# Kernel optimization log

Hardware: AMD Instinct MI355X
Metric: run time of the kernel (lower is better)

## Reference

```python
import jax, jax.numpy as jnp
import numpy as np

# BERT-base geometry
B, N, H, DH = 4, 512, 12, 64
HID = H * DH            # 768
E = 65536               # total edges (~avg degree 32)
NREL = 64               # relation vocabulary


def setup_inputs() -> dict:
    key = jax.random.key(0)
    ks = jax.random.split(key, 12)
    node_states = jax.random.normal(ks[0], (B, N, HID), jnp.float32)
    b = jax.random.randint(ks[1], (E,), 0, B)
    hn = jax.random.randint(ks[2], (E,), 0, N)
    tn = jax.random.randint(ks[3], (E,), 0, N)
    r = jax.random.randint(ks[4], (E,), 0, NREL)
    edge_indices = jnp.stack([b, hn, tn, r]).astype(jnp.int32)  # (4, E)
    node_type_ids = jnp.zeros((B, N), jnp.int32)  # unused by this subclass
    sc = 0.02
    Wq = jax.random.normal(ks[5], (HID, HID), jnp.float32) * sc
    bq = jnp.zeros((HID,), jnp.float32)
    Wk = jax.random.normal(ks[6], (HID, HID), jnp.float32) * sc
    bk = jnp.zeros((HID,), jnp.float32)
    Wv = jax.random.normal(ks[7], (HID, HID), jnp.float32) * sc
    bv = jnp.zeros((HID,), jnp.float32)
    # relation matrix embeddings: one (DH, DH) matrix per relation id
    rel_emb = jnp.eye(DH, dtype=jnp.float32)[None] + jax.random.normal(ks[8], (NREL, DH, DH), jnp.float32) * sc
    return {"node_states": node_states, "edge_indices": edge_indices,
            "node_type_ids": node_type_ids, "Wq": Wq, "bq": bq,
            "Wk": Wk, "bk": bk, "Wv": Wv, "bv": bv, "rel_emb": rel_emb}


def reference(node_states, edge_indices, node_type_ids, Wq, bq, Wk, bk, Wv, bv, rel_emb):
    Bq, Nn, hid = node_states.shape
    # dense QKV projections (torch Linear: y = x @ W^T + b)
    Q = node_states @ Wq.T + bq
    K = node_states @ Wk.T + bk
    V = (node_states @ Wv.T + bv).reshape(Bq, Nn, H, DH)  # (B,N,H,D)
    be, he, te, re = edge_indices  # each (E,)
    # per-edge gathers
    Qe = Q[be, he].reshape(-1, H, DH)   # (E,H,D)
    Ke = K[be, te].reshape(-1, H, DH)   # (E,H,D)
    Re = rel_emb[re]                     # (E,D,D) relation matrix per edge
    # Q projected through relation matrix, then inner product with K per head
    Qp = jnp.einsum('ehd,edk->ehk', Qe, Re)
    logits = jnp.einsum('ehd,ehd->eh', Qp, Ke) / jnp.sqrt(jnp.float32(DH))  # (E,H)
    # sparse softmax over tail nodes: segment = (batch, head_node)
    seg = be * Nn + he
    nseg = Bq * Nn
    m = jax.ops.segment_max(logits, seg, num_segments=nseg)      # (BN,H)
    ex = jnp.exp(logits - m[seg])
    denom = jax.ops.segment_sum(ex, seg, num_segments=nseg)      # (BN,H)
    p = ex / denom[seg]                                          # (E,H)
    # dropout prob = 0.0 (deterministic reference)
    # aggregate: out[b,i,h,:] = sum_edges p_e * V[b, tail_e, h, :]
    contrib = p[:, :, None] * V[be, te]                          # (E,H,D)
    out = jax.ops.segment_sum(contrib, seg, num_segments=nseg)   # (BN,H,D)
    return out.reshape(Bq, Nn, H * DH)
```

## Files before the change

kernel.cpp:

```cpp
#include <hip/hip_runtime.h>
#include <hip/hip_bf16.h>

#define NB   4
#define NN   512
#define NH   12
#define DHD  64
#define HID  768
#define NE   65536
#define NSEG 2048
#define NREL 64
#define NSUB 32
#define NRSUB (NREL * NSUB)
#define LGS  16
#define POISON 0xAAAAAAAAu

typedef short bf16x8 __attribute__((ext_vector_type(8)));
typedef float f32x4  __attribute__((ext_vector_type(4)));
typedef unsigned short u16x8 __attribute__((ext_vector_type(8)));

__device__ __forceinline__ unsigned short f2bf(float f) {
    __hip_bfloat16 h = __float2bfloat16(f);
    return *reinterpret_cast<unsigned short*>(&h);
}
__device__ __forceinline__ float bf2f(unsigned short s) {
    return __int_as_float(((int)s) << 16);
}
__device__ __forceinline__ int unpz(int v) {
    return (int)((unsigned)v - POISON);
}
__device__ __forceinline__ void load_lds16(const void* g, void* l) {
    __builtin_amdgcn_global_load_lds(
        (const __attribute__((address_space(1))) unsigned int*)g,
        (__attribute__((address_space(3))) unsigned int*)l, 16, 0, 0);
}

#define NX4 ((2048 * 768) / 4)
#define NW4 ((768 * 768) / 4)
#define NCAST ((NX4 + 3 * NW4) / 256)
__global__ __launch_bounds__(256) void cast_hist_kernel(
    const float* __restrict__ X, const float* __restrict__ Wq,
    const float* __restrict__ Wk, const float* __restrict__ Wv,
    unsigned short* __restrict__ Xh, unsigned short* __restrict__ Wh,
    const int* __restrict__ ei,
    int* __restrict__ count, int* __restrict__ rcount2)
{
    if (blockIdx.x >= NCAST) {
        const int e = (blockIdx.x - NCAST) * 256 + threadIdx.x;
        const int b  = ei[e];
        const int hn = ei[NE + e];
        const int rr = ei[3 * NE + e];
        const int sub = (e >> 8) & (NSUB - 1);
        atomicAdd(&count[b * NN + hn], 1);
        atomicAdd(&rcount2[rr * NSUB + sub], 1);
        return;
    }
    const int i = blockIdx.x * 256 + threadIdx.x;
    float4 v;
    ushort4* dst;
    if (i < NX4) {
        v = ((const float4*)X)[i];
        dst = &((ushort4*)Xh)[i];
    } else {
        const int j = i - NX4;
        const float* W = (j < NW4) ? Wq : ((j < 2 * NW4) ? Wk : Wv);
        const int jj = (j < NW4) ? j : ((j < 2 * NW4) ? j - NW4 : j - 2 * NW4);
        v = ((const float4*)W)[jj];
        dst = &((ushort4*)Wh)[j];
    }
    ushort4 r;
    r.x = f2bf(v.x); r.y = f2bf(v.y); r.z = f2bf(v.z); r.w = f2bf(v.w);
    *dst = r;
}

#define NQKV 576
__global__ __launch_bounds__(256) void qkv_scatter_kernel(
    const unsigned short* __restrict__ Xh, const unsigned short* __restrict__ Wh,
    const float* __restrict__ bq, const float* __restrict__ bk,
    const float* __restrict__ bv,
    unsigned short* __restrict__ Qh, unsigned short* __restrict__ Kh,
    unsigned short* __restrict__ Vh,
    const int* __restrict__ ei,
    const int* __restrict__ count, const int* __restrict__ rcount2,
    int* __restrict__ cursor, int* __restrict__ rcursor2,
    int* __restrict__ s_te, int* __restrict__ s_pk, int* __restrict__ r_pos,
    int* __restrict__ offs_g, int* __restrict__ rofs2_g)
{
    __shared__ __align__(16) char smem[64 * 132 * 4];
    const int tid = threadIdx.x;

    if (blockIdx.x >= NQKV) {
        int* offs_l = (int*)smem;
        int* rofs_l = offs_l + NSEG;
        int* buf    = rofs_l + NRSUB;
        int* extra  = buf + 256;

        {
            int local[8];
            int s = 0;
            #pragma unroll
            for (int i = 0; i < 8; ++i) { local[i] = unpz(count[tid * 8 + i]); s += local[i]; }
            buf[tid] = s;
            __syncthreads();
            for (int off = 1; off < 256; off <<= 1) {
                const int v = (tid >= off) ? buf[tid - off] : 0;
                __syncthreads();
                buf[tid] += v;
                __syncthreads();
            }
            int run = buf[tid] - s;
            #pragma unroll
            for (int i = 0; i < 8; ++i) { offs_l[tid * 8 + i] = run; run += local[i]; }
            if (tid == 255) extra[0] = run;
            __syncthreads();
        }
        {
            int local[8];
            int s = 0;
            #pragma unroll
            for (int i = 0; i < 8; ++i) { local[i] = unpz(rcount2[tid * 8 + i]); s += local[i]; }
            buf[tid] = s;
            __syncthreads();
            for (int off = 1; off < 256; off <<= 1) {
                const int v = (tid >= off) ? buf[tid - off] : 0;
                __syncthreads();
                buf[tid] += v;
                __syncthreads();
            }
            int run = buf[tid] - s;
            #pragma unroll
            for (int i = 0; i < 8; ++i) { rofs_l[tid * 8 + i] = run; run += local[i]; }
            if (blockIdx.x == NQKV && tid == 255) rofs2_g[NRSUB] = run;
        }
        __syncthreads();

        if (blockIdx.x == NQKV) {
            #pragma unroll
            for (int i = 0; i < 8; ++i) {
                offs_g[tid * 8 + i]  = offs_l[tid * 8 + i];
                rofs2_g[tid * 8 + i] = rofs_l[tid * 8 + i];
            }
            if (tid == 255) offs_g[NSEG] = extra[0];
        }

        const int e = (blockIdx.x - NQKV) * 256 + tid;
        const int b  = ei[e];
        const int hn = ei[NE + e];
        const int tn = ei[2 * NE + e];
        const int rr = ei[3 * NE + e];
        const int sub = (e >> 8) & (NSUB - 1);
        const int seg = b * NN + hn;
        const int pos = offs_l[seg] + unpz(atomicAdd(&cursor[seg], 1));
        s_te[pos] = tn;
        s_pk[pos] = (seg << 9) | tn;
        const int rb = rr * NSUB + sub;
        const int rj = unpz(atomicAdd(&rcursor2[rb], 1));
        r_pos[rofs_l[rb] + rj] = pos;
        return;
    }

    const int bid = blockIdx.x;
    const int z   = bid / 192;
    const int rem = bid - z * 192;
    const int by  = rem / 6;
    const int bx  = rem - by * 6;
    const unsigned short* W = Wh + (size_t)z * (768 * 768);
    const float* bias = (z == 0) ? bq : ((z == 1) ? bk : bv);

    const int n0 = bx * 128;
    const int m0 = by * 64;
    const int lane = tid & 63;
    const int wave = tid >> 6;
    const int wm = wave >> 1, wn = wave & 1;

    unsigned short* As = (unsigned short*)smem;
    unsigned short* Bs = (unsigned short*)(smem + 8192);
    float* Cs = (float*)smem;

    f32x4 acc[2][4];
    #pragma unroll
    for (int a = 0; a < 2; ++a)
        #pragma unroll
        for (int b2 = 0; b2 < 4; ++b2) acc[a][b2] = (f32x4){0.f, 0.f, 0.f, 0.f};

    const int ml = lane & 15;
    const int q4 = lane >> 4;

    for (int k0 = 0; k0 < HID; k0 += 64) {
        __syncthreads();
        #pragma unroll
        for (int i = 0; i < 2; ++i) {
            const int slotb = i * 256 + wave * 64;
            const int idx = slotb + lane;
            const int row = idx >> 3;
            const int kq  = (idx & 7) ^ (row & 7);
            load_lds16(Xh + (size_t)(m0 + row) * HID + k0 + kq * 8,
                       As + slotb * 8);
        }
        #pragma unroll
        for (int i = 0; i < 4; ++i) {
            const int slotb = i * 256 + wave * 64;
            const int idx = slotb + lane;
            const int row = idx >> 3;
            const int kq  = (idx & 7) ^ (row & 7);
            load_lds16(W + (size_t)(n0 + row) * HID + k0 + kq * 8,
                       Bs + slotb * 8);
        }
        __syncthreads();

        #pragma unroll
        for (int ks = 0; ks < 2; ++ks) {
            bf16x8 af[2], bfr[4];
            #pragma unroll
            for (int t = 0; t < 2; ++t) {
                const int ar = wm * 32 + t * 16 + ml;
                const int ac = (ks * 4 + q4) ^ (ar & 7);
                af[t] = *(const bf16x8*)(As + ar * 64 + ac * 8);
            }
            #pragma unroll
            for (int t = 0; t < 4; ++t) {
                const int br = wn * 64 + t * 16 + ml;
                const int bc = (ks * 4 + q4) ^ (br & 7);
                bfr[t] = *(const bf16x8*)(Bs + br * 64 + bc * 8);
            }
            #pragma unroll
            for (int mt = 0; mt < 2; ++mt)
                #pragma unroll
                for (int nt = 0; nt < 4; ++nt)
                    acc[mt][nt] = __builtin_amdgcn_mfma_f32_16x16x32_bf16(
                        af[mt], bfr[nt], acc[mt][nt], 0, 0, 0);
        }
    }

    __syncthreads();
    #pragma unroll
    for (int mt = 0; mt < 2; ++mt)
        #pragma unroll
        for (int nt = 0; nt < 4; ++nt)
            #pragma unroll
            for (int rg = 0; rg < 4; ++rg)
                Cs[(wm * 32 + mt * 16 + q4 * 4 + rg) * 132 +
                   wn * 64 + nt * 16 + ml] = acc[mt][nt][rg];
    __syncthreads();

    unsigned short* Y = (z == 0) ? Qh : ((z == 1) ? Kh : Vh);
    #pragma unroll
    for (int it = 0; it < 4; ++it) {
        const int id  = tid + it * 256;
        const int row = id >> 4;
        const int cg  = id & 15;
        const float* cp = Cs + row * 132 + cg * 8;
        const float4 cA = *(const float4*)cp;
        const float4 cB = *(const float4*)(cp + 4);
        const float* bp = bias + n0 + cg * 8;
        const float4 bA = *(const float4*)bp;
        const float4 bB = *(const float4*)(bp + 4);
        const size_t o = (size_t)(m0 + row) * HID + n0 + cg * 8;
        u16x8 r;
        r[0] = f2bf(cA.x + bA.x); r[1] = f2bf(cA.y + bA.y);
        r[2] = f2bf(cA.z + bA.z); r[3] = f2bf(cA.w + bA.w);
        r[4] = f2bf(cB.x + bB.x); r[5] = f2bf(cB.y + bB.y);
        r[6] = f2bf(cB.z + bB.z); r[7] = f2bf(cB.w + bB.w);
        *(u16x8*)&Y[o] = r;
    }
}

#define RLY 32
__global__ __launch_bounds__(256) void rel_logits(
    const unsigned short* __restrict__ Qh, const unsigned short* __restrict__ Kh,
    const float* __restrict__ rel,
    const int* __restrict__ rofs2, const int* __restrict__ r_pos,
    const int* __restrict__ s_pk,
    float* __restrict__ Lg)
{
    const int r = blockIdx.x;
    const int rstart = rofs2[r * NSUB];
    const int rows = (rofs2[(r + 1) * NSUB] - rstart) * NH;
    if ((int)blockIdx.y * 256 >= rows) return;
    const int tid = threadIdx.x;
    const int lane = tid & 63;
    const int wave = tid >> 6;

    __shared__ int qb[256], kb[256], oi[256];
    __shared__ float QpS[4][16][68];

    bf16x8 bfrag[2][4];
    {
        const float* Rg = rel + (size_t)r * 4096;
        const int q4 = lane >> 4, n = lane & 15;
        #pragma unroll
        for (int ks = 0; ks < 2; ++ks)
            #pragma unroll
            for (int nt = 0; nt < 4; ++nt) {
                bf16x8 f;
                #pragma unroll
                for (int j = 0; j < 8; ++j)
                    f[j] = (short)f2bf(Rg[(ks * 32 + q4 * 8 + j) * 64 + nt * 16 + n]);
                bfrag[ks][nt] = f;
            }
    }

    for (int t0 = blockIdx.y * 256; t0 < rows; t0 += RLY * 256) {
        __syncthreads();
        {
            const int rowid = t0 + tid;
            if (rowid < rows) {
                const int el = rowid / 12;
                const int h  = rowid - el * 12;
                const int pos = r_pos[rstart + el];
                const int pk  = s_pk[pos];
                const int seg = pk >> 9;
                const int te  = pk & (NN - 1);
                qb[tid] = seg * HID + h * 64;
                kb[tid] = ((seg & ~(NN - 1)) + te) * HID + h * 64;
                oi[tid] = pos * LGS + h;
            } else { qb[tid] = 0; kb[tid] = 0; oi[tid] = -1; }
        }
        __syncthreads();

        for (int g = wave; g < 16; g += 4) {
            const int m = lane & 15, q4 = lane >> 4;
            const int qbase = qb[g * 16 + m];
            f32x4 cfr[4] = {{0,0,0,0},{0,0,0,0},{0,0,0,0},{0,0,0,0}};
            #pragma unroll
            for (int ks = 0; ks < 2; ++ks) {
                const bf16x8 afr = *(const bf16x8*)(Qh + qbase + ks * 32 + q4 * 8);
                #pragma unroll
                for (int nt = 0; nt < 4; ++nt)
                    cfr[nt] = __builtin_amdgcn_mfma_f32_16x16x32_bf16(
                        afr, bfrag[ks][nt], cfr[nt], 0, 0, 0);
            }
            #pragma unroll
            for (int nt = 0; nt < 4; ++nt)
                #pragma unroll
                for (int rg = 0; rg < 4; ++rg)
                    QpS[wave][q4 * 4 + rg][nt * 16 + m] = cfr[nt][rg];

            const int rw = lane >> 2, ch = (lane & 3) * 16;
            const int rowid2 = g * 16 + rw;
            const int kbase = kb[rowid2];
            const bf16x8 k0 = *(const bf16x8*)(Kh + kbase + ch);
            const bf16x8 k1 = *(const bf16x8*)(Kh + kbase + ch + 8);
            float s = 0.f;
            #pragma unroll
            for (int i = 0; i < 8; ++i) {
                s = fmaf(QpS[wave][rw][ch + i],     bf2f((unsigned short)k0[i]), s);
                s = fmaf(QpS[wave][rw][ch + 8 + i], bf2f((unsigned short)k1[i]), s);
            }
            s += __shfl_xor(s, 1, 64);
            s += __shfl_xor(s, 2, 64);
            if ((lane & 3) == 0) {
                const int o = oi[rowid2];
                if (o >= 0) Lg[o] = __expf(s * 0.125f);
            }
        }
    }
}

__global__ __launch_bounds__(256) void seg_softmax_agg(
    const unsigned short* __restrict__ Vh, const float* __restrict__ Lg,
    const int* __restrict__ offs, const int* __restrict__ s_te,
    float* __restrict__ out)
{
    const int seg  = blockIdx.x;
    const int tid  = threadIdx.x;
    const int lane = tid & 63;
    const int w    = tid >> 6;
    const int start = offs[seg];
    const int cnt   = offs[seg + 1] - start;
    const int browbase = seg & ~(NN - 1);

    __shared__ int   te_s[64];
    __shared__ float pv[4][3][64];

    float l0 = 0.f, l1 = 0.f, l2 = 0.f;
    float acc0 = 0.f, acc1 = 0.f, acc2 = 0.f;

    for (int c0 = 0; c0 < cnt; c0 += 64) {
        const int cc = min(64, cnt - c0);
        __syncthreads();
        if (tid < cc) te_s[tid] = s_te[start + c0 + tid];
        __syncthreads();

        float p0 = 0.f, p1 = 0.f, p2 = 0.f;
        if (lane < cc) {
            const float* Lp = Lg + (size_t)(start + c0 + lane) * LGS;
            p0 = Lp[w]; p1 = Lp[4 + w]; p2 = Lp[8 + w];
        }
        float s0 = p0, s1 = p1, s2 = p2;
        #pragma unroll
        for (int o = 1; o < 64; o <<= 1) {
            s0 += __shfl_xor(s0, o, 64);
            s1 += __shfl_xor(s1, o, 64);
            s2 += __shfl_xor(s2, o, 64);
        }
        l0 += s0; l1 += s1; l2 += s2;
        pv[w][0][lane] = p0; pv[w][1][lane] = p1; pv[w][2][lane] = p2;

        for (int j = 0; j < cc; ++j) {
            const unsigned short* __restrict__ Vr =
                Vh + (size_t)(browbase + te_s[j]) * HID + lane;
            acc0 = fmaf(pv[w][0][j], bf2f(Vr[w * 64]),       acc0);
            acc1 = fmaf(pv[w][1][j], bf2f(Vr[(4 + w) * 64]), acc1);
            acc2 = fmaf(pv[w][2][j], bf2f(Vr[(8 + w) * 64]), acc2);
        }
    }

    float* Yo = out + (size_t)seg * HID;
    Yo[tid]       = (l0 > 0.f) ? acc0 / l0 : 0.f;
    Yo[tid + 256] = (l1 > 0.f) ? acc1 / l1 : 0.f;
    Yo[tid + 512] = (l2 > 0.f) ? acc2 / l2 : 0.f;
}

extern "C" void kernel_launch(void* const* d_in, const int* in_sizes, int n_in,
                              void* d_out, int out_size, void* d_ws, size_t ws_size,
                              hipStream_t stream)
{
    const float* X   = (const float*)d_in[0];
    const int*   EI  = (const int*)d_in[1];
    const float* Wq  = (const float*)d_in[3];
    const float* bq  = (const float*)d_in[4];
    const float* Wk  = (const float*)d_in[5];
    const float* bk  = (const float*)d_in[6];
    const float* Wv  = (const float*)d_in[7];
    const float* bv  = (const float*)d_in[8];
    const float* rel = (const float*)d_in[9];
    float* out = (float*)d_out;

    char* p = (char*)d_ws;
    unsigned short* Qh = (unsigned short*)p;  p += (size_t)NSEG * HID * 2;
    unsigned short* Kh = (unsigned short*)p;  p += (size_t)NSEG * HID * 2;
    unsigned short* Vh = (unsigned short*)p;  p += (size_t)NSEG * HID * 2;
    unsigned short* Xh = (unsigned short*)p;
    float* Lg = (float*)p;                    p += (size_t)NE * LGS * 4;
    unsigned short* Wh = (unsigned short*)p;  p += (size_t)3 * 768 * 768 * 2;
    int* offs     = (int*)p;                  p += 2052 * 4;
    int* rofs2    = (int*)p;                  p += (NRSUB + 4) * 4;
    int* count    = (int*)p;                  p += NSEG * 4;
    int* cursor   = (int*)p;                  p += NSEG * 4;
    int* rcount2  = (int*)p;                  p += NRSUB * 4;
    int* rcursor2 = (int*)p;                  p += NRSUB * 4;
    int* s_te     = (int*)p;                  p += NE * 4;
    int* s_pk     = (int*)p;                  p += NE * 4;
    int* r_pos    = (int*)p;                  p += NE * 4;

    cast_hist_kernel<<<NCAST + 256, 256, 0, stream>>>(
        X, Wq, Wk, Wv, Xh, Wh, EI, count, rcount2);
    qkv_scatter_kernel<<<NQKV + 256, 256, 0, stream>>>(
        Xh, Wh, bq, bk, bv, Qh, Kh, Vh,
        EI, count, rcount2, cursor, rcursor2, s_te, s_pk, r_pos, offs, rofs2);
    rel_logits<<<dim3(NREL, RLY), 256, 0, stream>>>(Qh, Kh, rel, rofs2, r_pos,
                                                    s_pk, Lg);
    seg_softmax_agg<<<NSEG, 256, 0, stream>>>(Vh, Lg, offs, s_te, out);
}
```

Measured before the change: 160.2 us.

## Store logits head-major and split aggregation edges across waves with vector V loads

The exponentiated logits buffer changes from a per-edge stride-16 layout to a head-major [head][edge] layout, so the softmax/aggregation kernel reads them with coalesced loads. The aggregation loop is also restructured. Each wave now takes every fourth edge and loads the full 768-wide V row with 4-element vector loads, where before every wave walked all edges with scalar 2-byte loads. Per-wave partial sums are then reduced through LDS, which costs an extra 12 KB of shared memory and an extra reduction and sync step at the end.

```diff
diff --git a/kernel.cpp b/kernel.cpp
--- a/kernel.cpp
+++ b/kernel.cpp
@@ -11,12 +11,12 @@
 #define NREL 64
 #define NSUB 32
 #define NRSUB (NREL * NSUB)
-#define LGS  16
 #define POISON 0xAAAAAAAAu
 
 typedef short bf16x8 __attribute__((ext_vector_type(8)));
 typedef float f32x4  __attribute__((ext_vector_type(4)));
 typedef unsigned short u16x8 __attribute__((ext_vector_type(8)));
+typedef unsigned short u16x4 __attribute__((ext_vector_type(4)));
 
 __device__ __forceinline__ unsigned short f2bf(float f) {
     __hip_bfloat16 h = __float2bfloat16(f);
@@ -312,7 +312,7 @@
                 const int te  = pk & (NN - 1);
                 qb[tid] = seg * HID + h * 64;
                 kb[tid] = ((seg & ~(NN - 1)) + te) * HID + h * 64;
-                oi[tid] = pos * LGS + h;
+                oi[tid] = h * NE + pos;
             } else { qb[tid] = 0; kb[tid] = 0; oi[tid] = -1; }
         }
         __syncthreads();
@@ -365,26 +365,34 @@
     const int tid  = threadIdx.x;
     const int lane = tid & 63;
     const int w    = tid >> 6;
+    const int hq   = lane >> 4;
     const int start = offs[seg];
     const int cnt   = offs[seg + 1] - start;
     const int browbase = seg & ~(NN - 1);
 
     __shared__ int   te_s[64];
     __shared__ float pv[4][3][64];
+    __shared__ float accS[4][768];
+    __shared__ float ls[16];
 
     float l0 = 0.f, l1 = 0.f, l2 = 0.f;
-    float acc0 = 0.f, acc1 = 0.f, acc2 = 0.f;
+    float acc[3][4];
+    #pragma unroll
+    for (int k = 0; k < 3; ++k)
+        #pragma unroll
+        for (int t = 0; t < 4; ++t) acc[k][t] = 0.f;
 
     for (int c0 = 0; c0 < cnt; c0 += 64) {
         const int cc = min(64, cnt - c0);
         __syncthreads();
         if (tid < cc) te_s[tid] = s_te[start + c0 + tid];
-        __syncthreads();
 
         float p0 = 0.f, p1 = 0.f, p2 = 0.f;
         if (lane < cc) {
-            const float* Lp = Lg + (size_t)(start + c0 + lane) * LGS;
-            p0 = Lp[w]; p1 = Lp[4 + w]; p2 = Lp[8 + w];
+            const int gi = start + c0 + lane;
+            p0 = Lg[w * NE + gi];
+            p1 = Lg[(4 + w) * NE + gi];
+            p2 = Lg[(8 + w) * NE + gi];
         }
         float s0 = p0, s1 = p1, s2 = p2;
         #pragma unroll
@@ -395,20 +403,43 @@
         }
         l0 += s0; l1 += s1; l2 += s2;
         pv[w][0][lane] = p0; pv[w][1][lane] = p1; pv[w][2][lane] = p2;
-
-        for (int j = 0; j < cc; ++j) {
+        __syncthreads();
+
+        for (int j = w; j < cc; j += 4) {
             const unsigned short* __restrict__ Vr =
-                Vh + (size_t)(browbase + te_s[j]) * HID + lane;
-            acc0 = fmaf(pv[w][0][j], bf2f(Vr[w * 64]),       acc0);
-            acc1 = fmaf(pv[w][1][j], bf2f(Vr[(4 + w) * 64]), acc1);
-            acc2 = fmaf(pv[w][2][j], bf2f(Vr[(8 + w) * 64]), acc2);
-        }
-    }
+                Vh + (size_t)(browbase + te_s[j]) * HID + lane * 4;
+            const float pa0 = pv[hq][0][j];
+            const float pa1 = pv[hq][1][j];
+            const float pa2 = pv[hq][2][j];
+            const u16x4 v0 = *(const u16x4*)(Vr);
+            const u16x4 v1 = *(const u16x4*)(Vr + 256);
+            const u16x4 v2 = *(const u16x4*)(Vr + 512);
+            #pragma unroll
+            for (int t = 0; t < 4; ++t) {
+                acc[0][t] = fmaf(pa0, bf2f(v0[t]), acc[0][t]);
+                acc[1][t] = fmaf(pa1, bf2f(v1[t]), acc[1][t]);
+                acc[2][t] = fmaf(pa2, bf2f(v2[t]), acc[2][t]);
+            }
+        }
+    }
+
+    __syncthreads();
+    #pragma unroll
+    for (int k = 0; k < 3; ++k)
+        #pragma unroll
+        for (int t = 0; t < 4; ++t)
+            accS[w][k * 256 + lane * 4 + t] = acc[k][t];
+    if (lane == 0) { ls[w] = l0; ls[4 + w] = l1; ls[8 + w] = l2; }
+    __syncthreads();
 
     float* Yo = out + (size_t)seg * HID;
-    Yo[tid]       = (l0 > 0.f) ? acc0 / l0 : 0.f;
-    Yo[tid + 256] = (l1 > 0.f) ? acc1 / l1 : 0.f;
-    Yo[tid + 512] = (l2 > 0.f) ? acc2 / l2 : 0.f;
+    #pragma unroll
+    for (int k = 0; k < 3; ++k) {
+        const int d = k * 256 + tid;
+        const float sum = accS[0][d] + accS[1][d] + accS[2][d] + accS[3][d];
+        const float l = ls[d >> 6];
+        Yo[d] = (l > 0.f) ? sum / l : 0.f;
+    }
 }
 
 extern "C" void kernel_launch(void* const* d_in, const int* in_sizes, int n_in,
@@ -431,7 +462,7 @@
     unsigned short* Kh = (unsigned short*)p;  p += (size_t)NSEG * HID * 2;
     unsigned short* Vh = (unsigned short*)p;  p += (size_t)NSEG * HID * 2;
     unsigned short* Xh = (unsigned short*)p;
-    float* Lg = (float*)p;                    p += (size_t)NE * LGS * 4;
+    float* Lg = (float*)p;                    p += (size_t)NH * NE * 4;
     unsigned short* Wh = (unsigned short*)p;  p += (size_t)3 * 768 * 768 * 2;
     int* offs     = (int*)p;                  p += 2052 * 4;
     int* rofs2    = (int*)p;                  p += (NRSUB + 4) * 4;
```

New measurement: 162.9 us. No clear change (+1.7%).
